# Kernel optimization log

Hardware: AMD Instinct MI355X
Metric: run time of the kernel (lower is better)

Reference implementation:

```python
import jax, jax.numpy as jnp
import numpy as np

N = 50000
E = 800000
D = 128
H = 128
C = 2
NUM_GRAPHS = 512
EPS = 1e-5


def setup_inputs() -> dict:
    key = jax.random.key(0)
    ks = jax.random.split(key, 12)
    x = jax.random.normal(ks[0], (N, D), dtype=jnp.float32)
    edge_index = jax.random.randint(ks[1], (2, E), 0, N, dtype=jnp.int64)
    batch = jnp.sort(jax.random.randint(ks[2], (N,), 0, NUM_GRAPHS, dtype=jnp.int64))
    s = 1.0 / np.sqrt(D)
    w1l = jax.random.uniform(ks[3], (D, H), jnp.float32, -s, s)
    w1r = jax.random.uniform(ks[4], (D, H), jnp.float32, -s, s)
    b1 = jax.random.uniform(ks[5], (H,), jnp.float32, -s, s)
    sh = 1.0 / np.sqrt(H)
    w2l = jax.random.uniform(ks[6], (H, H), jnp.float32, -sh, sh)
    w2r = jax.random.uniform(ks[7], (H, H), jnp.float32, -sh, sh)
    b2 = jax.random.uniform(ks[8], (H,), jnp.float32, -sh, sh)
    gamma1 = jnp.ones((H,), jnp.float32)
    beta1 = jnp.zeros((H,), jnp.float32)
    gamma2 = jnp.ones((H,), jnp.float32)
    beta2 = jnp.zeros((H,), jnp.float32)
    wlin = jax.random.uniform(ks[9], (H, C), jnp.float32, -sh, sh)
    blin = jax.random.uniform(ks[10], (C,), jnp.float32, -sh, sh)
    return {"x": x, "edge_index": edge_index, "batch": batch,
            "w1l": w1l, "w1r": w1r, "b1": b1, "gamma1": gamma1, "beta1": beta1,
            "w2l": w2l, "w2r": w2r, "b2": b2, "gamma2": gamma2, "beta2": beta2,
            "wlin": wlin, "blin": blin}


def _sage_conv(x, src, dst, wl, wr, b):
    # mean-aggregate source features at target nodes, then linear
    agg = jax.ops.segment_sum(x[src], dst, num_segments=N)          # [N, F]
    cnt = jax.ops.segment_sum(jnp.ones((src.shape[0],), x.dtype), dst, num_segments=N)
    agg = agg / jnp.maximum(cnt, 1.0)[:, None]
    return agg @ wl + b + x @ wr


def _batch_norm(x, gamma, beta):
    mu = jnp.mean(x, axis=0)
    var = jnp.mean(jnp.square(x - mu), axis=0)  # biased, as torch BN training
    return (x - mu) * (gamma / jnp.sqrt(var + EPS)) + beta


def reference(x, edge_index, batch, w1l, w1r, b1, gamma1, beta1,
              w2l, w2r, b2, gamma2, beta2, wlin, blin):
    src, dst = edge_index[0], edge_index[1]
    h = _sage_conv(x, src, dst, w1l, w1r, b1)
    h = jax.nn.relu(_batch_norm(h, gamma1, beta1))
    h = _sage_conv(h, src, dst, w2l, w2r, b2)
    h = jax.nn.relu(_batch_norm(h, gamma2, beta2))
    # global mean pool over graphs
    pooled = jax.ops.segment_sum(h, batch, num_segments=NUM_GRAPHS)
    cnt = jax.ops.segment_sum(jnp.ones((N,), h.dtype), batch, num_segments=NUM_GRAPHS)
    pooled = pooled / jnp.maximum(cnt, 1.0)[:, None]
    return jax.nn.sigmoid(pooled @ wlin + blin)
```

## Files before the change

kernel.cpp:

```cpp
#include <hip/hip_runtime.h>

#define N_NODES 50000
#define N_EDGES 800000
#define NGRAPH 512
#define MAXDEG 64
#define BN_EPS 1e-5f
#define NTILES 3125

typedef __attribute__((ext_vector_type(8))) short s16x8;
typedef __attribute__((ext_vector_type(4))) float f32x4;

__device__ __forceinline__ ushort bf16_rne(float f) {
  uint u = __float_as_uint(f);
  return (ushort)((u + 0x7FFFu + ((u >> 16) & 1u)) >> 16);
}
__device__ __forceinline__ void bf16split(float f, ushort& h, ushort& l) {
  uint u = __float_as_uint(f);
  uint hb = (u + 0x7FFFu + ((u >> 16) & 1u)) & 0xFFFF0000u;
  h = (ushort)(hb >> 16);
  l = bf16_rne(f - __uint_as_float(hb));
}
__device__ __forceinline__ float bf16f(ushort h) {
  return __uint_as_float(((uint)h) << 16);
}
__device__ __forceinline__ void acc_pk(float* a, uint4 v) {
  a[0] += __uint_as_float(v.x << 16);
  a[1] += __uint_as_float(v.x & 0xFFFF0000u);
  a[2] += __uint_as_float(v.y << 16);
  a[3] += __uint_as_float(v.y & 0xFFFF0000u);
  a[4] += __uint_as_float(v.z << 16);
  a[5] += __uint_as_float(v.z & 0xFFFF0000u);
  a[6] += __uint_as_float(v.w << 16);
  a[7] += __uint_as_float(v.w & 0xFFFF0000u);
}

__global__ __launch_bounds__(256) void fill_kernel(
    const int* __restrict__ ei, int* __restrict__ cursor, ushort* __restrict__ csr)
{
  int e = blockIdx.x * 256 + threadIdx.x;
  if (e < N_EDGES) {
    int dst = ei[N_EDGES + e];
    int slot = atomicAdd(&cursor[dst], 1);
    if (slot < MAXDEG) csr[dst * MAXDEG + slot] = (ushort)ei[e];
  }
}

__global__ __launch_bounds__(256) void wpack_kernel(
    const float* __restrict__ w1l, const float* __restrict__ w1r,
    const float* __restrict__ w2l, const float* __restrict__ w2r,
    ushort* __restrict__ Wph, ushort* __restrict__ Wpl)
{
  int idx = blockIdx.x * 256 + threadIdx.x;
  int layer = idx >> 15;
  int e = idx & 32767;
  int j = e & 7, l = (e >> 3) & 63, t = (e >> 9) & 7, s = e >> 12;
  int k = s * 32 + ((l >> 4) << 3) + j;
  int col = t * 16 + (l & 15);
  const float* wl = layer ? w2l : w1l;
  const float* wr = layer ? w2r : w1r;
  float w = (k < 128) ? wl[k * 128 + col] : wr[(k - 128) * 128 + col];
  ushort h, lo;
  bf16split(w, h, lo);
  Wph[idx] = h;
  Wpl[idx] = lo;
}

__global__ __launch_bounds__(256) void splitx_kernel(
    const float* __restrict__ x, ushort* __restrict__ Ahi)
{
  int i = blockIdx.x * 256 + threadIdx.x;
  if (i >= N_NODES * 32) return;
  int n = i >> 5, j = i & 31;
  float4 v = ((const float4*)x)[i];
  ushort4 h;
  h.x = bf16_rne(v.x); h.y = bf16_rne(v.y);
  h.z = bf16_rne(v.z); h.w = bf16_rne(v.w);
  *(ushort4*)(Ahi + (size_t)n * 256 + 128 + j * 4) = h;
}

__global__ __launch_bounds__(256) void gather_kernel(
    ushort* Ahi,
    const ushort* __restrict__ csr, const int* __restrict__ deg)
{
  int gid = blockIdx.x * 256 + threadIdx.x;
  int n = gid >> 4, j = gid & 15;
  if (n >= N_NODES) return;
  int d = min(deg[n], MAXDEG);
  const ushort* lst = csr + n * MAXDEG;
  float a[8] = {0.f, 0.f, 0.f, 0.f, 0.f, 0.f, 0.f, 0.f};
  int i = 0;
  for (; i + 4 <= d; i += 4) {
    int s0 = lst[i], s1 = lst[i + 1], s2 = lst[i + 2], s3 = lst[i + 3];
    uint4 h0 = *(const uint4*)(Ahi + (size_t)s0 * 256 + 128 + j * 8);
    uint4 h1 = *(const uint4*)(Ahi + (size_t)s1 * 256 + 128 + j * 8);
    uint4 h2 = *(const uint4*)(Ahi + (size_t)s2 * 256 + 128 + j * 8);
    uint4 h3 = *(const uint4*)(Ahi + (size_t)s3 * 256 + 128 + j * 8);
    acc_pk(a, h0); acc_pk(a, h1); acc_pk(a, h2); acc_pk(a, h3);
  }
  for (; i < d; ++i) {
    uint4 h = *(const uint4*)(Ahi + (size_t)lst[i] * 256 + 128 + j * 8);
    acc_pk(a, h);
  }
  float inv = 1.0f / fmaxf((float)d, 1.0f);
  ushort hh[8];
  #pragma unroll
  for (int k = 0; k < 8; ++k) {
    a[k] *= inv;
    hh[k] = bf16_rne(a[k]);
  }
  uint4 ho;
  ho.x = (uint)hh[0] | ((uint)hh[1] << 16);
  ho.y = (uint)hh[2] | ((uint)hh[3] << 16);
  ho.z = (uint)hh[4] | ((uint)hh[5] << 16);
  ho.w = (uint)hh[6] | ((uint)hh[7] << 16);
  *(uint4*)(Ahi + (size_t)n * 256 + j * 8) = ho;
}

__global__ __launch_bounds__(512) void gemm_kernel(
    const ushort* __restrict__ Ahi,
    const ushort* __restrict__ Wph, const ushort* __restrict__ Wpl,
    const float* __restrict__ bias,
    float* __restrict__ z, float* __restrict__ stats)
{
  __shared__ uint4 lds_w[8192];
  __shared__ float lds_stats[256];
  int tid = threadIdx.x;

  {
    const uint4* gh = (const uint4*)Wph;
    const uint4* gl = (const uint4*)Wpl;
    #pragma unroll
    for (int i = 0; i < 8; ++i) lds_w[tid + i * 512] = gh[tid + i * 512];
    #pragma unroll
    for (int i = 0; i < 8; ++i) lds_w[4096 + tid + i * 512] = gl[tid + i * 512];
  }
  if (tid < 256) lds_stats[tid] = 0.f;
  __syncthreads();

  int wave = tid >> 6, lane = tid & 63;
  int col0 = lane & 15, rg = lane >> 4;
  int t0 = blockIdx.x * 16 + wave * 2;
  bool v0 = t0 < NTILES, v1 = (t0 + 1) < NTILES;
  int r0 = min(t0 * 16 + col0, N_NODES - 1);
  int r1 = min(t0 * 16 + 16 + col0, N_NODES - 1);

  const s16x8* W8h = (const s16x8*)lds_w;
  const s16x8* W8l = W8h + 4096;
  const s16x8* pah0 = (const s16x8*)Ahi + (size_t)r0 * 32 + rg;
  const s16x8* pah1 = (const s16x8*)Ahi + (size_t)r1 * 32 + rg;

  f32x4 acc0[8], acc1[8];
  #pragma unroll
  for (int t = 0; t < 8; ++t) {
    float bc = bias[t * 16 + col0];
    acc0[t] = (f32x4){bc, bc, bc, bc};
    acc1[t] = acc0[t];
  }

  for (int s = 0; s < 8; ++s) {
    s16x8 ah0 = pah0[s * 4];
    s16x8 ah1 = pah1[s * 4];
    #pragma unroll
    for (int t = 0; t < 8; ++t) {
      s16x8 wh = W8h[(s * 8 + t) * 64 + lane];
      s16x8 wo = W8l[(s * 8 + t) * 64 + lane];
      acc0[t] = __builtin_amdgcn_mfma_f32_16x16x32_bf16(ah0, wh, acc0[t], 0, 0, 0);
      acc0[t] = __builtin_amdgcn_mfma_f32_16x16x32_bf16(ah0, wo, acc0[t], 0, 0, 0);
      acc1[t] = __builtin_amdgcn_mfma_f32_16x16x32_bf16(ah1, wh, acc1[t], 0, 0, 0);
      acc1[t] = __builtin_amdgcn_mfma_f32_16x16x32_bf16(ah1, wo, acc1[t], 0, 0, 0);
    }
  }

  float psum[8], psq[8];
  #pragma unroll
  for (int t = 0; t < 8; ++t) { psum[t] = 0.f; psq[t] = 0.f; }
  if (v0) {
    #pragma unroll
    for (int t = 0; t < 8; ++t) {
      #pragma unroll
      for (int r = 0; r < 4; ++r) {
        float v = acc0[t][r];
        z[(size_t)(t0 * 16 + rg * 4 + r) * 128 + t * 16 + col0] = v;
        psum[t] += v; psq[t] += v * v;
      }
    }
  }
  if (v1) {
    #pragma unroll
    for (int t = 0; t < 8; ++t) {
      #pragma unroll
      for (int r = 0; r < 4; ++r) {
        float v = acc1[t][r];
        z[(size_t)(t0 * 16 + 16 + rg * 4 + r) * 128 + t * 16 + col0] = v;
        psum[t] += v; psq[t] += v * v;
      }
    }
  }

  #pragma unroll
  for (int t = 0; t < 8; ++t) {
    atomicAdd(&lds_stats[t * 16 + col0], psum[t]);
    atomicAdd(&lds_stats[128 + t * 16 + col0], psq[t]);
  }
  __syncthreads();
  if (tid < 256) atomicAdd(&stats[tid], lds_stats[tid]);
}

__global__ __launch_bounds__(128) void finalize_kernel(
    const float* __restrict__ stats, const float* __restrict__ gamma,
    const float* __restrict__ beta, float* __restrict__ scsh)
{
  int f = threadIdx.x;
  const float invN = 1.0f / (float)N_NODES;
  float mu = stats[f] * invN;
  float var = stats[128 + f] * invN - mu * mu;
  var = fmaxf(var, 0.f);
  float s = gamma[f] * rsqrtf(var + BN_EPS);
  scsh[f] = s;
  scsh[128 + f] = beta[f] - mu * s;
}

__global__ __launch_bounds__(256) void bnrelu_split_kernel(
    const float* __restrict__ z, const float* __restrict__ scsh,
    ushort* __restrict__ Ahi)
{
  const float4* sc4 = (const float4*)scsh;
  const float4* sh4 = (const float4*)(scsh + 128);
  int i = blockIdx.x * 256 + threadIdx.x;
  if (i >= N_NODES * 32) return;
  int n = i >> 5, c4 = i & 31;
  float4 v = ((const float4*)z)[i];
  float4 s = sc4[c4], hh = sh4[c4];
  v.x = fmaxf(0.f, fmaf(v.x, s.x, hh.x));
  v.y = fmaxf(0.f, fmaf(v.y, s.y, hh.y));
  v.z = fmaxf(0.f, fmaf(v.z, s.z, hh.z));
  v.w = fmaxf(0.f, fmaf(v.w, s.w, hh.w));
  ushort4 h;
  h.x = bf16_rne(v.x); h.y = bf16_rne(v.y);
  h.z = bf16_rne(v.z); h.w = bf16_rne(v.w);
  *(ushort4*)(Ahi + (size_t)n * 256 + 128 + c4 * 4) = h;
}

__global__ __launch_bounds__(256) void bnrelu_kernel(
    float* __restrict__ z, const float* __restrict__ scsh)
{
  const float4* sc4 = (const float4*)scsh;
  const float4* sh4 = (const float4*)(scsh + 128);
  int i = blockIdx.x * 256 + threadIdx.x;
  if (i >= N_NODES * 32) return;
  int c4 = i & 31;
  float4 v = ((float4*)z)[i];
  float4 s = sc4[c4], h = sh4[c4];
  v.x = fmaxf(0.f, fmaf(v.x, s.x, h.x));
  v.y = fmaxf(0.f, fmaf(v.y, s.y, h.y));
  v.z = fmaxf(0.f, fmaf(v.z, s.z, h.z));
  v.w = fmaxf(0.f, fmaf(v.w, s.w, h.w));
  ((float4*)z)[i] = v;
}

__global__ __launch_bounds__(256) void bounds_kernel(
    const int* __restrict__ batch, int* __restrict__ starts)
{
  int g = blockIdx.x * 256 + threadIdx.x;
  if (g > NGRAPH) return;
  int lo = 0, hi = N_NODES;
  while (lo < hi) {
    int mid = (lo + hi) >> 1;
    if (batch[mid] < g) lo = mid + 1; else hi = mid;
  }
  starts[g] = lo;
}

__global__ __launch_bounds__(256) void pool_head_kernel(
    const float* __restrict__ h, const int* __restrict__ starts,
    const float* __restrict__ wlin, const float* __restrict__ blin,
    float* __restrict__ out)
{
  __shared__ float pl[256];
  __shared__ float s0[128];
  __shared__ float s1[128];
  int g = blockIdx.x;
  int tid = threadIdx.x;
  int f = tid & 127, half = tid >> 7;
  int start = starts[g], end = starts[g + 1];
  int cnt = end - start;

  float acc = 0.f;
  int r = start + half;
  for (; r + 8 <= end; r += 8) {
    float v0 = h[(size_t)r * 128 + f];
    float v1 = h[(size_t)(r + 2) * 128 + f];
    float v2 = h[(size_t)(r + 4) * 128 + f];
    float v3 = h[(size_t)(r + 6) * 128 + f];
    acc += (v0 + v1) + (v2 + v3);
  }
  for (; r < end; r += 2) acc += h[(size_t)r * 128 + f];

  pl[tid] = acc;
  __syncthreads();
  if (tid < 128) {
    float inv = 1.0f / fmaxf((float)cnt, 1.0f);
    float p = (pl[tid] + pl[tid + 128]) * inv;
    s0[tid] = p * wlin[tid * 2 + 0];
    s1[tid] = p * wlin[tid * 2 + 1];
  }
  __syncthreads();
  if (tid < 64) {
    float a0 = s0[tid] + s0[tid + 64];
    float a1 = s1[tid] + s1[tid + 64];
    for (int off = 32; off > 0; off >>= 1) {
      a0 += __shfl_down(a0, off, 64);
      a1 += __shfl_down(a1, off, 64);
    }
    if (tid == 0) {
      out[g * 2 + 0] = 1.0f / (1.0f + expf(-(a0 + blin[0])));
      out[g * 2 + 1] = 1.0f / (1.0f + expf(-(a1 + blin[1])));
    }
  }
}

extern "C" void kernel_launch(void* const* d_in, const int* in_sizes, int n_in,
                              void* d_out, int out_size, void* d_ws, size_t ws_size,
                              hipStream_t stream) {
  const float* x    = (const float*)d_in[0];
  const int*   ei   = (const int*)d_in[1];
  const int*   batch= (const int*)d_in[2];
  const float* w1l  = (const float*)d_in[3];
  const float* w1r  = (const float*)d_in[4];
  const float* b1   = (const float*)d_in[5];
  const float* g1   = (const float*)d_in[6];
  const float* be1  = (const float*)d_in[7];
  const float* w2l  = (const float*)d_in[8];
  const float* w2r  = (const float*)d_in[9];
  const float* b2   = (const float*)d_in[10];
  const float* g2   = (const float*)d_in[11];
  const float* be2  = (const float*)d_in[12];
  const float* wlin = (const float*)d_in[13];
  const float* blin = (const float*)d_in[14];
  float* out = (float*)d_out;

  char* ws = (char*)d_ws;
  int*    cursor = (int*)(ws + 0);
  ushort* csr    = (ushort*)(ws + 400000);
  ushort* Ahi    = (ushort*)(ws + 6800000);
  float*  z      = (float*)(ws + 58000000);
  float*  stats  = (float*)(ws + 83600000);
  float*  scsh   = stats + 256;
  int*    starts = (int*)(scsh + 256);
  ushort* Wph    = (ushort*)(ws + 83866240);
  ushort* Wpl    = (ushort*)(ws + 83997312);

  const int eblocks = (N_EDGES + 255) / 256;
  const int nblocks = (N_NODES * 32 + 255) / 256;
  const int gblocks = (N_NODES * 16 + 255) / 256;
  const int gemmblocks = (NTILES + 15) / 16;

  hipMemsetAsync(cursor, 0, N_NODES * sizeof(int), stream);
  fill_kernel<<<eblocks, 256, 0, stream>>>(ei, cursor, csr);
  wpack_kernel<<<256, 256, 0, stream>>>(w1l, w1r, w2l, w2r, Wph, Wpl);
  bounds_kernel<<<3, 256, 0, stream>>>(batch, starts);

  splitx_kernel<<<nblocks, 256, 0, stream>>>(x, Ahi);
  gather_kernel<<<gblocks, 256, 0, stream>>>(Ahi, csr, cursor);
  hipMemsetAsync(stats, 0, 256 * 4, stream);
  gemm_kernel<<<gemmblocks, 512, 0, stream>>>(Ahi, Wph, Wpl, b1, z, stats);
  finalize_kernel<<<1, 128, 0, stream>>>(stats, g1, be1, scsh);
  bnrelu_split_kernel<<<nblocks, 256, 0, stream>>>(z, scsh, Ahi);

  gather_kernel<<<gblocks, 256, 0, stream>>>(Ahi, csr, cursor);
  hipMemsetAsync(stats, 0, 256 * 4, stream);
  gemm_kernel<<<gemmblocks, 512, 0, stream>>>(Ahi, Wph + 32768, Wpl + 32768, b2, z, stats);
  finalize_kernel<<<1, 128, 0, stream>>>(stats, g2, be2, scsh);
  bnrelu_kernel<<<nblocks, 256, 0, stream>>>(z, scsh);

  pool_head_kernel<<<NGRAPH, 256, 0, stream>>>(z, starts, wlin, blin, out);
}
```

Baseline: 211.2 us.

## Store GEMM output as bf16, fuse final BN-ReLU into pooling, merge setup kernels

The GEMM now writes its pre-BN output as bf16 instead of fp32, halving z write and read traffic. The final BN+ReLU pass is folded into the pooling head, which reads bf16 z and applies scale/shift on the fly. The bounds search is merged into the weight-pack kernel as an extra block, and the stats memsets are folded into the cursor memset by relocating stats. This removes several launches and passes but rounds z to bf16 before BN, adding precision loss.

Result: no change. 207.2 us (-1.9%).

```diff
diff --git a/kernel.cpp b/kernel.cpp
--- a/kernel.cpp
+++ b/kernel.cpp
@@ -19,9 +19,6 @@
   uint hb = (u + 0x7FFFu + ((u >> 16) & 1u)) & 0xFFFF0000u;
   h = (ushort)(hb >> 16);
   l = bf16_rne(f - __uint_as_float(hb));
-}
-__device__ __forceinline__ float bf16f(ushort h) {
-  return __uint_as_float(((uint)h) << 16);
 }
 __device__ __forceinline__ void acc_pk(float* a, uint4 v) {
   a[0] += __uint_as_float(v.x << 16);
@@ -45,11 +42,23 @@
   }
 }
 
-__global__ __launch_bounds__(256) void wpack_kernel(
+__global__ __launch_bounds__(256) void wpack_bounds_kernel(
     const float* __restrict__ w1l, const float* __restrict__ w1r,
     const float* __restrict__ w2l, const float* __restrict__ w2r,
-    ushort* __restrict__ Wph, ushort* __restrict__ Wpl)
-{
+    ushort* __restrict__ Wph, ushort* __restrict__ Wpl,
+    const int* __restrict__ batch, int* __restrict__ starts)
+{
+  if (blockIdx.x == 256) {
+    for (int g = threadIdx.x; g <= NGRAPH; g += 256) {
+      int lo = 0, hi = N_NODES;
+      while (lo < hi) {
+        int mid = (lo + hi) >> 1;
+        if (batch[mid] < g) lo = mid + 1; else hi = mid;
+      }
+      starts[g] = lo;
+    }
+    return;
+  }
   int idx = blockIdx.x * 256 + threadIdx.x;
   int layer = idx >> 15;
   int e = idx & 32767;
@@ -120,7 +129,7 @@
     const ushort* __restrict__ Ahi,
     const ushort* __restrict__ Wph, const ushort* __restrict__ Wpl,
     const float* __restrict__ bias,
-    float* __restrict__ z, float* __restrict__ stats)
+    ushort* __restrict__ zb, float* __restrict__ stats)
 {
   __shared__ uint4 lds_w[8192];
   __shared__ float lds_stats[256];
@@ -180,7 +189,7 @@
       #pragma unroll
       for (int r = 0; r < 4; ++r) {
         float v = acc0[t][r];
-        z[(size_t)(t0 * 16 + rg * 4 + r) * 128 + t * 16 + col0] = v;
+        zb[(size_t)(t0 * 16 + rg * 4 + r) * 128 + t * 16 + col0] = bf16_rne(v);
         psum[t] += v; psq[t] += v * v;
       }
     }
@@ -191,7 +200,7 @@
       #pragma unroll
       for (int r = 0; r < 4; ++r) {
         float v = acc1[t][r];
-        z[(size_t)(t0 * 16 + 16 + rg * 4 + r) * 128 + t * 16 + col0] = v;
+        zb[(size_t)(t0 * 16 + 16 + rg * 4 + r) * 128 + t * 16 + col0] = bf16_rne(v);
         psum[t] += v; psq[t] += v * v;
       }
     }
@@ -221,100 +230,76 @@
 }
 
 __global__ __launch_bounds__(256) void bnrelu_split_kernel(
-    const float* __restrict__ z, const float* __restrict__ scsh,
+    const ushort* __restrict__ zb, const float* __restrict__ scsh,
     ushort* __restrict__ Ahi)
 {
-  const float4* sc4 = (const float4*)scsh;
-  const float4* sh4 = (const float4*)(scsh + 128);
   int i = blockIdx.x * 256 + threadIdx.x;
-  if (i >= N_NODES * 32) return;
-  int n = i >> 5, c4 = i & 31;
-  float4 v = ((const float4*)z)[i];
-  float4 s = sc4[c4], hh = sh4[c4];
-  v.x = fmaxf(0.f, fmaf(v.x, s.x, hh.x));
-  v.y = fmaxf(0.f, fmaf(v.y, s.y, hh.y));
-  v.z = fmaxf(0.f, fmaf(v.z, s.z, hh.z));
-  v.w = fmaxf(0.f, fmaf(v.w, s.w, hh.w));
-  ushort4 h;
-  h.x = bf16_rne(v.x); h.y = bf16_rne(v.y);
-  h.z = bf16_rne(v.z); h.w = bf16_rne(v.w);
-  *(ushort4*)(Ahi + (size_t)n * 256 + 128 + c4 * 4) = h;
-}
-
-__global__ __launch_bounds__(256) void bnrelu_kernel(
-    float* __restrict__ z, const float* __restrict__ scsh)
-{
-  const float4* sc4 = (const float4*)scsh;
-  const float4* sh4 = (const float4*)(scsh + 128);
-  int i = blockIdx.x * 256 + threadIdx.x;
-  if (i >= N_NODES * 32) return;
-  int c4 = i & 31;
-  float4 v = ((float4*)z)[i];
-  float4 s = sc4[c4], h = sh4[c4];
-  v.x = fmaxf(0.f, fmaf(v.x, s.x, h.x));
-  v.y = fmaxf(0.f, fmaf(v.y, s.y, h.y));
-  v.z = fmaxf(0.f, fmaf(v.z, s.z, h.z));
-  v.w = fmaxf(0.f, fmaf(v.w, s.w, h.w));
-  ((float4*)z)[i] = v;
-}
-
-__global__ __launch_bounds__(256) void bounds_kernel(
-    const int* __restrict__ batch, int* __restrict__ starts)
-{
-  int g = blockIdx.x * 256 + threadIdx.x;
-  if (g > NGRAPH) return;
-  int lo = 0, hi = N_NODES;
-  while (lo < hi) {
-    int mid = (lo + hi) >> 1;
-    if (batch[mid] < g) lo = mid + 1; else hi = mid;
-  }
-  starts[g] = lo;
+  if (i >= N_NODES * 16) return;
+  int n = i >> 4, g8 = i & 15;
+  uint4 v = *(const uint4*)(zb + (size_t)n * 128 + g8 * 8);
+  float4 sA = *(const float4*)(scsh + g8 * 8);
+  float4 sB = *(const float4*)(scsh + g8 * 8 + 4);
+  float4 tA = *(const float4*)(scsh + 128 + g8 * 8);
+  float4 tB = *(const float4*)(scsh + 128 + g8 * 8 + 4);
+  float z0 = __uint_as_float(v.x << 16), z1 = __uint_as_float(v.x & 0xFFFF0000u);
+  float z2 = __uint_as_float(v.y << 16), z3 = __uint_as_float(v.y & 0xFFFF0000u);
+  float z4 = __uint_as_float(v.z << 16), z5 = __uint_as_float(v.z & 0xFFFF0000u);
+  float z6 = __uint_as_float(v.w << 16), z7 = __uint_as_float(v.w & 0xFFFF0000u);
+  z0 = fmaxf(0.f, fmaf(z0, sA.x, tA.x));
+  z1 = fmaxf(0.f, fmaf(z1, sA.y, tA.y));
+  z2 = fmaxf(0.f, fmaf(z2, sA.z, tA.z));
+  z3 = fmaxf(0.f, fmaf(z3, sA.w, tA.w));
+  z4 = fmaxf(0.f, fmaf(z4, sB.x, tB.x));
+  z5 = fmaxf(0.f, fmaf(z5, sB.y, tB.y));
+  z6 = fmaxf(0.f, fmaf(z6, sB.z, tB.z));
+  z7 = fmaxf(0.f, fmaf(z7, sB.w, tB.w));
+  uint4 o;
+  o.x = (uint)bf16_rne(z0) | ((uint)bf16_rne(z1) << 16);
+  o.y = (uint)bf16_rne(z2) | ((uint)bf16_rne(z3) << 16);
+  o.z = (uint)bf16_rne(z4) | ((uint)bf16_rne(z5) << 16);
+  o.w = (uint)bf16_rne(z6) | ((uint)bf16_rne(z7) << 16);
+  *(uint4*)(Ahi + (size_t)n * 256 + 128 + g8 * 8) = o;
 }
 
 __global__ __launch_bounds__(256) void pool_head_kernel(
-    const float* __restrict__ h, const int* __restrict__ starts,
+    const ushort* __restrict__ zb, const int* __restrict__ starts,
+    const float* __restrict__ scsh,
     const float* __restrict__ wlin, const float* __restrict__ blin,
     float* __restrict__ out)
 {
-  __shared__ float pl[256];
-  __shared__ float s0[128];
-  __shared__ float s1[128];
+  __shared__ float pl0[256], pl1[256];
   int g = blockIdx.x;
   int tid = threadIdx.x;
-  int f = tid & 127, half = tid >> 7;
+  int p = tid & 63;
+  int h4 = tid >> 6;
   int start = starts[g], end = starts[g + 1];
   int cnt = end - start;
-
-  float acc = 0.f;
-  int r = start + half;
-  for (; r + 8 <= end; r += 8) {
-    float v0 = h[(size_t)r * 128 + f];
-    float v1 = h[(size_t)(r + 2) * 128 + f];
-    float v2 = h[(size_t)(r + 4) * 128 + f];
-    float v3 = h[(size_t)(r + 6) * 128 + f];
-    acc += (v0 + v1) + (v2 + v3);
-  }
-  for (; r < end; r += 2) acc += h[(size_t)r * 128 + f];
-
-  pl[tid] = acc;
-  __syncthreads();
-  if (tid < 128) {
-    float inv = 1.0f / fmaxf((float)cnt, 1.0f);
-    float p = (pl[tid] + pl[tid + 128]) * inv;
-    s0[tid] = p * wlin[tid * 2 + 0];
-    s1[tid] = p * wlin[tid * 2 + 1];
-  }
+  float s0 = scsh[2 * p],       s1 = scsh[2 * p + 1];
+  float t0 = scsh[128 + 2 * p], t1 = scsh[128 + 2 * p + 1];
+  float a0 = 0.f, a1 = 0.f;
+  for (int r = start + h4; r < end; r += 4) {
+    uint v = *(const uint*)(zb + (size_t)r * 128 + p * 2);
+    float z0 = __uint_as_float(v << 16);
+    float z1 = __uint_as_float(v & 0xFFFF0000u);
+    a0 += fmaxf(0.f, fmaf(z0, s0, t0));
+    a1 += fmaxf(0.f, fmaf(z1, s1, t1));
+  }
+  pl0[tid] = a0;
+  pl1[tid] = a1;
   __syncthreads();
   if (tid < 64) {
-    float a0 = s0[tid] + s0[tid + 64];
-    float a1 = s1[tid] + s1[tid + 64];
+    float inv = 1.0f / fmaxf((float)cnt, 1.0f);
+    float p0 = (pl0[tid] + pl0[tid + 64] + pl0[tid + 128] + pl0[tid + 192]) * inv;
+    float p1 = (pl1[tid] + pl1[tid + 64] + pl1[tid + 128] + pl1[tid + 192]) * inv;
+    float b0 = fmaf(p0, wlin[(2 * tid) * 2 + 0], p1 * wlin[(2 * tid + 1) * 2 + 0]);
+    float b1 = fmaf(p0, wlin[(2 * tid) * 2 + 1], p1 * wlin[(2 * tid + 1) * 2 + 1]);
     for (int off = 32; off > 0; off >>= 1) {
-      a0 += __shfl_down(a0, off, 64);
-      a1 += __shfl_down(a1, off, 64);
+      b0 += __shfl_down(b0, off, 64);
+      b1 += __shfl_down(b1, off, 64);
     }
     if (tid == 0) {
-      out[g * 2 + 0] = 1.0f / (1.0f + expf(-(a0 + blin[0])));
-      out[g * 2 + 1] = 1.0f / (1.0f + expf(-(a1 + blin[1])));
+      out[g * 2 + 0] = 1.0f / (1.0f + expf(-(b0 + blin[0])));
+      out[g * 2 + 1] = 1.0f / (1.0f + expf(-(b1 + blin[1])));
     }
   }
 }
@@ -341,37 +326,36 @@
 
   char* ws = (char*)d_ws;
   int*    cursor = (int*)(ws + 0);
+  float*  stats  = (float*)(ws + 200000);
+  float*  scsh   = (float*)(ws + 202048);
+  int*    starts = (int*)(ws + 203072);
   ushort* csr    = (ushort*)(ws + 400000);
   ushort* Ahi    = (ushort*)(ws + 6800000);
-  float*  z      = (float*)(ws + 58000000);
-  float*  stats  = (float*)(ws + 83600000);
-  float*  scsh   = stats + 256;
-  int*    starts = (int*)(scsh + 256);
+  ushort* zb     = (ushort*)(ws + 58000000);
   ushort* Wph    = (ushort*)(ws + 83866240);
   ushort* Wpl    = (ushort*)(ws + 83997312);
 
   const int eblocks = (N_EDGES + 255) / 256;
   const int nblocks = (N_NODES * 32 + 255) / 256;
   const int gblocks = (N_NODES * 16 + 255) / 256;
+  const int bblocks = (N_NODES * 16 + 255) / 256;
   const int gemmblocks = (NTILES + 15) / 16;
 
-  hipMemsetAsync(cursor, 0, N_NODES * sizeof(int), stream);
+  hipMemsetAsync(cursor, 0, 202048, stream);
   fill_kernel<<<eblocks, 256, 0, stream>>>(ei, cursor, csr);
-  wpack_kernel<<<256, 256, 0, stream>>>(w1l, w1r, w2l, w2r, Wph, Wpl);
-  bounds_kernel<<<3, 256, 0, stream>>>(batch, starts);
+  wpack_bounds_kernel<<<257, 256, 0, stream>>>(w1l, w1r, w2l, w2r, Wph, Wpl,
+                                               batch, starts);
 
   splitx_kernel<<<nblocks, 256, 0, stream>>>(x, Ahi);
   gather_kernel<<<gblocks, 256, 0, stream>>>(Ahi, csr, cursor);
-  hipMemsetAsync(stats, 0, 256 * 4, stream);
-  gemm_kernel<<<gemmblocks, 512, 0, stream>>>(Ahi, Wph, Wpl, b1, z, stats);
+  gemm_kernel<<<gemmblocks, 512, 0, stream>>>(Ahi, Wph, Wpl, b1, zb, stats);
   finalize_kernel<<<1, 128, 0, stream>>>(stats, g1, be1, scsh);
-  bnrelu_split_kernel<<<nblocks, 256, 0, stream>>>(z, scsh, Ahi);
+  bnrelu_split_kernel<<<bblocks, 256, 0, stream>>>(zb, scsh, Ahi);
 
   gather_kernel<<<gblocks, 256, 0, stream>>>(Ahi, csr, cursor);
-  hipMemsetAsync(stats, 0, 256 * 4, stream);
-  gemm_kernel<<<gemmblocks, 512, 0, stream>>>(Ahi, Wph + 32768, Wpl + 32768, b2, z, stats);
-  finalize_kernel<<<1, 128, 0, stream>>>(stats, g2, be2, scsh);
-  bnrelu_kernel<<<nblocks, 256, 0, stream>>>(z, scsh);
-
-  pool_head_kernel<<<NGRAPH, 256, 0, stream>>>(z, starts, wlin, blin, out);
-}
+  gemm_kernel<<<gemmblocks, 512, 0, stream>>>(Ahi, Wph + 32768, Wpl + 32768, b2,
+                                              zb, stats + 256);
+  finalize_kernel<<<1, 128, 0, stream>>>(stats + 256, g2, be2, scsh);
+
+  pool_head_kernel<<<NGRAPH, 256, 0, stream>>>(zb, starts, scsh, wlin, blin, out);
+}
```
